# Optimization experiments

Hardware: AMD Instinct MI355X
Metric: run time of the kernel (lower is better)

## Reference

```python
import jax, jax.numpy as jnp
import numpy as np

FACTOR = 1.0
KERNEL = 3
PAD = 1
STRIDE = 1


def setup_inputs() -> dict:
    key = jax.random.key(0)
    ks = jax.random.split(key, 7)
    B_, Cin, Cout, L, CODE = 32, 128, 128, 4096, 2
    return {
        "input": jax.random.normal(ks[0], (B_, Cin, L), dtype=jnp.float32),
        "codes": jax.random.normal(ks[1], (B_, CODE, CODE), dtype=jnp.float32),
        "weight": jax.random.normal(ks[2], (Cout, Cin, KERNEL), dtype=jnp.float32) * 0.05,
        "A": jax.random.normal(ks[3], (Cin, CODE, KERNEL), dtype=jnp.float32) * 0.05,
        "B": jax.random.normal(ks[4], (Cout, CODE, KERNEL), dtype=jnp.float32) * 0.05,
        "bias": jax.random.normal(ks[5], (Cout,), dtype=jnp.float32) * 0.05,
        "bias_context": jax.random.normal(ks[6], (CODE, Cout), dtype=jnp.float32) * 0.05,
    }


def reference(input, codes, weight, A, B, bias, bias_context):
    # Hypernetwork-generated per-sample conv weights (low-rank via codes)
    w = jnp.einsum('ick,bcr->birk', A, codes)            # (b, in, code, k)
    context_w = jnp.einsum('birk,ork->boik', w, B)       # (b, out, in, k)
    combined_weight = weight + FACTOR * context_w        # (b, out, in, k)

    diag = jnp.diagonal(codes, axis1=-2, axis2=-1)       # (b, code)
    context_bias = diag @ bias_context                   # (b, out)
    combined_bias = bias + FACTOR * context_bias         # (b, out)

    # circular padding along spatial axis
    padded = jnp.pad(input, ((0, 0), (0, 0), (PAD, PAD)), mode='wrap')
    L_out = (input.shape[-1] + 2 * PAD - KERNEL) // STRIDE + 1
    # windowed view: (b, in, L_out, k) via k shifted slices (k is tiny, loop ok)
    windows = jnp.stack([padded[:, :, j:j + L_out * STRIDE:STRIDE] for j in range(KERNEL)], axis=-1)
    out = jnp.einsum('bihw,boiw->boh', windows, combined_weight)
    return out + combined_bias[..., None]
```

## Files before the change

kernel.cpp:

```cpp
#include <hip/hip_runtime.h>
#include <hip/hip_bf16.h>
#include <stdint.h>
#include <stddef.h>

#define L_LEN 4096
#define CIN   128
#define COUT  128
#define NB    32
#define KTOT  384
#define TN    128
#define ROWS  (TN + 2)

typedef __bf16 bf16x8 __attribute__((ext_vector_type(8)));
typedef float  f32x4  __attribute__((ext_vector_type(4)));

__device__ __forceinline__ uint16_t f2bf(float f) {
    union { float f; uint32_t u; } v; v.f = f;
    return (uint16_t)((v.u + 0x7fffu + ((v.u >> 16) & 1u)) >> 16);
}
__device__ __forceinline__ uint32_t pack2(float lo, float hi) {
    return (uint32_t)f2bf(lo) | ((uint32_t)f2bf(hi) << 16);
}

__global__ __launch_bounds__(256) void geps_combine(
    const float* __restrict__ codes, const float* __restrict__ weight,
    const float* __restrict__ Amat,  const float* __restrict__ Bmat,
    const float* __restrict__ bias,  const float* __restrict__ bias_ctx,
    uint16_t* __restrict__ Wc, float* __restrict__ cbias)
{
    int tid = blockIdx.x * 256 + threadIdx.x;
    if (tid < NB * COUT * KTOT) {
        int b   = tid / (COUT * KTOT);
        int rem = tid % (COUT * KTOT);
        int o   = rem / KTOT;
        int kp  = rem % KTOT;
        int k   = kp >> 7;
        int i   = kp & 127;
        float cw = 0.f;
        #pragma unroll
        for (int c = 0; c < 2; ++c) {
            float a = Amat[i * 6 + c * 3 + k];
            #pragma unroll
            for (int r = 0; r < 2; ++r)
                cw += a * codes[b * 4 + c * 2 + r] * Bmat[o * 6 + r * 3 + k];
        }
        float val = weight[o * 384 + i * 3 + k] + cw;
        Wc[tid] = f2bf(val);
    }
    if (tid < NB * COUT) {
        int b = tid >> 7, o = tid & 127;
        float cb = bias[o];
        #pragma unroll
        for (int c = 0; c < 2; ++c)
            cb += codes[b * 4 + c * 2 + c] * bias_ctx[c * 128 + o];
        cbias[tid] = cb;
    }
}

__global__ __launch_bounds__(256, 4) void geps_conv(
    const float* __restrict__ in, const uint16_t* __restrict__ Wc,
    const float* __restrict__ cbias, float* __restrict__ out)
{
    __shared__ uint16_t __attribute__((aligned(16))) Xt[ROWS * 128];
    __shared__ float cb[COUT];

    const int tid  = threadIdx.x;
    const int b    = blockIdx.y;
    const int h0   = blockIdx.x * TN;
    const int lane = tid & 63;
    const int wid  = tid >> 6;

    if (tid < COUT) cb[tid] = cbias[b * COUT + tid];

    const float* inb = in + (size_t)b * CIN * L_LEN;

    #pragma unroll
    for (int it = 0; it < 8; ++it) {
        int task = it * 256 + tid;
        int p    = task >> 5;
        int qd   = task & 31;
        const float* r0 = inb + (size_t)(2 * p) * L_LEN + h0 + 4 * qd;
        const float4 a  = *(const float4*)r0;
        const float4 c  = *(const float4*)(r0 + L_LEN);
        const int off   = (2 * p) & 7;
        const int pc    = p >> 2;
        const float av[4] = {a.x, a.y, a.z, a.w};
        const float cv[4] = {c.x, c.y, c.z, c.w};
        #pragma unroll
        for (int j = 0; j < 4; ++j) {
            int r = 1 + 4 * qd + j;
            int chunk = pc ^ (r & 15);
            *(uint32_t*)&Xt[r * 128 + (chunk << 3) + off] = pack2(av[j], cv[j]);
        }
    }
    if (tid < 128) {
        int p    = tid & 63;
        int side = tid >> 6;
        int r    = side ? (ROWS - 1) : 0;
        int gh   = (h0 - 1 + r) & (L_LEN - 1);
        float x0 = inb[(size_t)(2 * p)     * L_LEN + gh];
        float x1 = inb[(size_t)(2 * p + 1) * L_LEN + gh];
        int chunk = (p >> 2) ^ (r & 15);
        *(uint32_t*)&Xt[r * 128 + (chunk << 3) + ((2 * p) & 7)] = pack2(x0, x1);
    }

    const int mq  = (wid & 1) * 64;
    const int nq  = (wid >> 1) * 64;
    const int m16 = lane & 15;
    const int q   = lane >> 4;

    f32x4 acc[4][4];
    #pragma unroll
    for (int a = 0; a < 4; ++a)
        #pragma unroll
        for (int c = 0; c < 4; ++c) acc[a][c] = 0.0f;

    const uint16_t* WcB = Wc + (size_t)b * COUT * KTOT;

    __syncthreads();

    #pragma unroll
    for (int t = 0; t < 12; ++t) {
        const int k   = t >> 2;
        const int i0c = (t & 3) * 4;
        bf16x8 af[4], bf[4];
        #pragma unroll
        for (int mt = 0; mt < 4; ++mt) {
            int o = mq + mt * 16 + m16;
            af[mt] = *(const bf16x8*)(WcB + (size_t)o * KTOT + t * 32 + q * 8);
        }
        #pragma unroll
        for (int nt = 0; nt < 4; ++nt) {
            int r  = nq + nt * 16 + m16 + k;
            int ch = (i0c + q) ^ (r & 15);
            bf[nt] = *(const bf16x8*)&Xt[r * 128 + (ch << 3)];
        }
        #pragma unroll
        for (int mt = 0; mt < 4; ++mt)
            #pragma unroll
            for (int nt = 0; nt < 4; ++nt)
                acc[mt][nt] = __builtin_amdgcn_mfma_f32_16x16x32_bf16(
                    af[mt], bf[nt], acc[mt][nt], 0, 0, 0);
    }

    float* outb = out + (size_t)b * COUT * L_LEN + h0;
    #pragma unroll
    for (int mt = 0; mt < 4; ++mt) {
        #pragma unroll
        for (int reg = 0; reg < 4; ++reg) {
            int o = mq + mt * 16 + q * 4 + reg;
            float bv = cb[o];
            float* orow = outb + (size_t)o * L_LEN;
            #pragma unroll
            for (int nt = 0; nt < 4; ++nt) {
                int h = nq + nt * 16 + m16;
                orow[h] = acc[mt][nt][reg] + bv;
            }
        }
    }
}

extern "C" void kernel_launch(void* const* d_in, const int* in_sizes, int n_in,
                              void* d_out, int out_size, void* d_ws, size_t ws_size,
                              hipStream_t stream) {
    const float* input    = (const float*)d_in[0];
    const float* codes    = (const float*)d_in[1];
    const float* weight   = (const float*)d_in[2];
    const float* Amat     = (const float*)d_in[3];
    const float* Bmat     = (const float*)d_in[4];
    const float* bias     = (const float*)d_in[5];
    const float* bias_ctx = (const float*)d_in[6];
    float* out = (float*)d_out;

    uint16_t* Wc    = (uint16_t*)d_ws;
    float*    cbias = (float*)((char*)d_ws + (size_t)NB * COUT * KTOT * 2);

    geps_combine<<<dim3((NB * COUT * KTOT) / 256), 256, 0, stream>>>(
        codes, weight, Amat, Bmat, bias, bias_ctx, Wc, cbias);
    geps_conv<<<dim3(L_LEN / TN, NB), 256, 0, stream>>>(input, Wc, cbias, out);
}
```

Baseline: 145.6 us.

## Prefetch full weight slice into registers and repartition warps over output rows

Each wave now owns 32 output channels across all 128 positions rather than a 64x64 quadrant. All 12 K-steps of its weight fragments are loaded into registers up front, before the input staging, so global weight latency overlaps the LDS fill. The input staging loads four channel rows per thread and writes 64-bit LDS stores instead of 32-bit ones. Occupancy hint drops from 4 to 2 blocks per CU to make room for the larger register footprint. The risk is lower occupancy hiding less of the memory latency.

```diff
diff --git a/kernel.cpp b/kernel.cpp
--- a/kernel.cpp
+++ b/kernel.cpp
@@ -57,7 +57,7 @@
     }
 }
 
-__global__ __launch_bounds__(256, 4) void geps_conv(
+__global__ __launch_bounds__(256, 2) void geps_conv(
     const float* __restrict__ in, const uint16_t* __restrict__ Wc,
     const float* __restrict__ cbias, float* __restrict__ out)
 {
@@ -69,28 +69,47 @@
     const int h0   = blockIdx.x * TN;
     const int lane = tid & 63;
     const int wid  = tid >> 6;
+    const int m16  = lane & 15;
+    const int q    = lane >> 4;
+    const int mq   = wid * 32;
 
     if (tid < COUT) cb[tid] = cbias[b * COUT + tid];
 
-    const float* inb = in + (size_t)b * CIN * L_LEN;
+    const uint16_t* WcB = Wc + (size_t)b * COUT * KTOT;
+    const float*    inb = in + (size_t)b * CIN * L_LEN;
+
+    bf16x8 af[12][2];
+    #pragma unroll
+    for (int t = 0; t < 12; ++t)
+        #pragma unroll
+        for (int mt = 0; mt < 2; ++mt)
+            af[t][mt] = *(const bf16x8*)(WcB +
+                (size_t)(mq + mt * 16 + m16) * KTOT + t * 32 + q * 8);
 
     #pragma unroll
-    for (int it = 0; it < 8; ++it) {
+    for (int it = 0; it < 4; ++it) {
         int task = it * 256 + tid;
-        int p    = task >> 5;
+        int p4   = task >> 5;
         int qd   = task & 31;
-        const float* r0 = inb + (size_t)(2 * p) * L_LEN + h0 + 4 * qd;
-        const float4 a  = *(const float4*)r0;
-        const float4 c  = *(const float4*)(r0 + L_LEN);
-        const int off   = (2 * p) & 7;
-        const int pc    = p >> 2;
-        const float av[4] = {a.x, a.y, a.z, a.w};
-        const float cv[4] = {c.x, c.y, c.z, c.w};
+        const float* r0 = inb + (size_t)(4 * p4) * L_LEN + h0 + 4 * qd;
+        float4 a0 = *(const float4*)(r0);
+        float4 a1 = *(const float4*)(r0 + L_LEN);
+        float4 a2 = *(const float4*)(r0 + 2 * L_LEN);
+        float4 a3 = *(const float4*)(r0 + 3 * L_LEN);
+        const int off = (4 * p4) & 7;
+        const int pc  = p4 >> 1;
+        const float v0[4] = {a0.x, a0.y, a0.z, a0.w};
+        const float v1[4] = {a1.x, a1.y, a1.z, a1.w};
+        const float v2[4] = {a2.x, a2.y, a2.z, a2.w};
+        const float v3[4] = {a3.x, a3.y, a3.z, a3.w};
         #pragma unroll
         for (int j = 0; j < 4; ++j) {
-            int r = 1 + 4 * qd + j;
-            int chunk = pc ^ (r & 15);
-            *(uint32_t*)&Xt[r * 128 + (chunk << 3) + off] = pack2(av[j], cv[j]);
+            int r  = 1 + 4 * qd + j;
+            int ch = pc ^ (r & 15);
+            uint2 w;
+            w.x = pack2(v0[j], v1[j]);
+            w.y = pack2(v2[j], v3[j]);
+            *(uint2*)&Xt[r * 128 + (ch << 3) + off] = w;
         }
     }
     if (tid < 128) {
@@ -104,18 +123,11 @@
         *(uint32_t*)&Xt[r * 128 + (chunk << 3) + ((2 * p) & 7)] = pack2(x0, x1);
     }
 
-    const int mq  = (wid & 1) * 64;
-    const int nq  = (wid >> 1) * 64;
-    const int m16 = lane & 15;
-    const int q   = lane >> 4;
-
-    f32x4 acc[4][4];
+    f32x4 acc[2][8];
     #pragma unroll
-    for (int a = 0; a < 4; ++a)
+    for (int a = 0; a < 2; ++a)
         #pragma unroll
-        for (int c = 0; c < 4; ++c) acc[a][c] = 0.0f;
-
-    const uint16_t* WcB = Wc + (size_t)b * COUT * KTOT;
+        for (int c = 0; c < 8; ++c) acc[a][c] = 0.0f;
 
     __syncthreads();
 
@@ -123,37 +135,32 @@
     for (int t = 0; t < 12; ++t) {
         const int k   = t >> 2;
         const int i0c = (t & 3) * 4;
-        bf16x8 af[4], bf[4];
+        bf16x8 bf[8];
         #pragma unroll
-        for (int mt = 0; mt < 4; ++mt) {
-            int o = mq + mt * 16 + m16;
-            af[mt] = *(const bf16x8*)(WcB + (size_t)o * KTOT + t * 32 + q * 8);
-        }
-        #pragma unroll
-        for (int nt = 0; nt < 4; ++nt) {
-            int r  = nq + nt * 16 + m16 + k;
+        for (int nt = 0; nt < 8; ++nt) {
+            int r  = nt * 16 + m16 + k;
             int ch = (i0c + q) ^ (r & 15);
             bf[nt] = *(const bf16x8*)&Xt[r * 128 + (ch << 3)];
         }
         #pragma unroll
-        for (int mt = 0; mt < 4; ++mt)
+        for (int mt = 0; mt < 2; ++mt)
             #pragma unroll
-            for (int nt = 0; nt < 4; ++nt)
+            for (int nt = 0; nt < 8; ++nt)
                 acc[mt][nt] = __builtin_amdgcn_mfma_f32_16x16x32_bf16(
-                    af[mt], bf[nt], acc[mt][nt], 0, 0, 0);
+                    af[t][mt], bf[nt], acc[mt][nt], 0, 0, 0);
     }
 
     float* outb = out + (size_t)b * COUT * L_LEN + h0;
     #pragma unroll
-    for (int mt = 0; mt < 4; ++mt) {
+    for (int mt = 0; mt < 2; ++mt) {
         #pragma unroll
         for (int reg = 0; reg < 4; ++reg) {
             int o = mq + mt * 16 + q * 4 + reg;
             float bv = cb[o];
             float* orow = outb + (size_t)o * L_LEN;
             #pragma unroll
-            for (int nt = 0; nt < 4; ++nt) {
-                int h = nq + nt * 16 + m16;
+            for (int nt = 0; nt < 8; ++nt) {
+                int h = nt * 16 + m16;
                 orow[h] = acc[mt][nt][reg] + bv;
             }
         }
```

Result: faster. 140.7 us (-3.4%).

## Pre-swizzle combined weights into MFMA fragment order and shrink spatial tile

Applied to the files above, without the earlier changes.

The combine kernel now writes the per-sample bf16 weights directly in MFMA A-fragment order, so each lane in the conv kernel loads its fragment with one contiguous, fully coalesced 16-byte read. The conv tile shrinks from 128 to 32 positions, each warp owns 32 output channels over all 32 positions, and launch bounds allow 8 blocks per CU. The goal is more blocks, higher occupancy and cheaper weight loads. In exchange, each block reloads the whole weight slice for only 32 positions, so weight traffic goes up about fourfold and each warp gets less MFMA reuse.

```diff
diff --git a/kernel.cpp b/kernel.cpp
--- a/kernel.cpp
+++ b/kernel.cpp
@@ -8,7 +8,7 @@
 #define COUT  128
 #define NB    32
 #define KTOT  384
-#define TN    128
+#define TN    32
 #define ROWS  (TN + 2)
 
 typedef __bf16 bf16x8 __attribute__((ext_vector_type(8)));
@@ -26,16 +26,20 @@
     const float* __restrict__ codes, const float* __restrict__ weight,
     const float* __restrict__ Amat,  const float* __restrict__ Bmat,
     const float* __restrict__ bias,  const float* __restrict__ bias_ctx,
-    uint16_t* __restrict__ Wc, float* __restrict__ cbias)
+    uint16_t* __restrict__ Wc2, float* __restrict__ cbias)
 {
     int tid = blockIdx.x * 256 + threadIdx.x;
     if (tid < NB * COUT * KTOT) {
-        int b   = tid / (COUT * KTOT);
-        int rem = tid % (COUT * KTOT);
-        int o   = rem / KTOT;
-        int kp  = rem % KTOT;
-        int k   = kp >> 7;
-        int i   = kp & 127;
+        int j    = tid & 7;
+        int lane = (tid >> 3) & 63;
+        int og   = (tid >> 9) & 7;
+        int x    = tid >> 12;
+        int b    = x / 12;
+        int t    = x - b * 12;
+        int o    = og * 16 + (lane & 15);
+        int kap  = t * 32 + (lane >> 4) * 8 + j;
+        int k    = kap >> 7;
+        int i    = kap & 127;
         float cw = 0.f;
         #pragma unroll
         for (int c = 0; c < 2; ++c) {
@@ -44,8 +48,7 @@
             for (int r = 0; r < 2; ++r)
                 cw += a * codes[b * 4 + c * 2 + r] * Bmat[o * 6 + r * 3 + k];
         }
-        float val = weight[o * 384 + i * 3 + k] + cw;
-        Wc[tid] = f2bf(val);
+        Wc2[tid] = f2bf(weight[o * 384 + i * 3 + k] + cw);
     }
     if (tid < NB * COUT) {
         int b = tid >> 7, o = tid & 127;
@@ -57,8 +60,8 @@
     }
 }
 
-__global__ __launch_bounds__(256, 4) void geps_conv(
-    const float* __restrict__ in, const uint16_t* __restrict__ Wc,
+__global__ __launch_bounds__(256, 8) void geps_conv(
+    const float* __restrict__ in, const uint16_t* __restrict__ Wc2,
     const float* __restrict__ cbias, float* __restrict__ out)
 {
     __shared__ uint16_t __attribute__((aligned(16))) Xt[ROWS * 128];
@@ -69,16 +72,19 @@
     const int h0   = blockIdx.x * TN;
     const int lane = tid & 63;
     const int wid  = tid >> 6;
+    const int m16  = lane & 15;
+    const int q    = lane >> 4;
+    const int mq   = wid * 32;
 
     if (tid < COUT) cb[tid] = cbias[b * COUT + tid];
 
     const float* inb = in + (size_t)b * CIN * L_LEN;
 
     #pragma unroll
-    for (int it = 0; it < 8; ++it) {
+    for (int it = 0; it < 2; ++it) {
         int task = it * 256 + tid;
-        int p    = task >> 5;
-        int qd   = task & 31;
+        int p    = task >> 3;
+        int qd   = task & 7;
         const float* r0 = inb + (size_t)(2 * p) * L_LEN + h0 + 4 * qd;
         const float4 a  = *(const float4*)r0;
         const float4 c  = *(const float4*)(r0 + L_LEN);
@@ -88,9 +94,9 @@
         const float cv[4] = {c.x, c.y, c.z, c.w};
         #pragma unroll
         for (int j = 0; j < 4; ++j) {
-            int r = 1 + 4 * qd + j;
-            int chunk = pc ^ (r & 15);
-            *(uint32_t*)&Xt[r * 128 + (chunk << 3) + off] = pack2(av[j], cv[j]);
+            int r  = 1 + 4 * qd + j;
+            int ch = pc ^ (r & 15);
+            *(uint32_t*)&Xt[r * 128 + (ch << 3) + off] = pack2(av[j], cv[j]);
         }
     }
     if (tid < 128) {
@@ -100,62 +106,53 @@
         int gh   = (h0 - 1 + r) & (L_LEN - 1);
         float x0 = inb[(size_t)(2 * p)     * L_LEN + gh];
         float x1 = inb[(size_t)(2 * p + 1) * L_LEN + gh];
-        int chunk = (p >> 2) ^ (r & 15);
-        *(uint32_t*)&Xt[r * 128 + (chunk << 3) + ((2 * p) & 7)] = pack2(x0, x1);
+        int ch   = (p >> 2) ^ (r & 15);
+        *(uint32_t*)&Xt[r * 128 + (ch << 3) + ((2 * p) & 7)] = pack2(x0, x1);
     }
 
-    const int mq  = (wid & 1) * 64;
-    const int nq  = (wid >> 1) * 64;
-    const int m16 = lane & 15;
-    const int q   = lane >> 4;
+    f32x4 acc[2][2];
+    #pragma unroll
+    for (int a = 0; a < 2; ++a)
+        #pragma unroll
+        for (int c = 0; c < 2; ++c) acc[a][c] = 0.0f;
 
-    f32x4 acc[4][4];
-    #pragma unroll
-    for (int a = 0; a < 4; ++a)
-        #pragma unroll
-        for (int c = 0; c < 4; ++c) acc[a][c] = 0.0f;
-
-    const uint16_t* WcB = Wc + (size_t)b * COUT * KTOT;
+    const uint16_t* afb = Wc2 + ((((size_t)b * 12) * 8 + wid * 2) << 9) + lane * 8;
 
     __syncthreads();
 
-    #pragma unroll
+    #pragma unroll 2
     for (int t = 0; t < 12; ++t) {
         const int k   = t >> 2;
         const int i0c = (t & 3) * 4;
-        bf16x8 af[4], bf[4];
+        bf16x8 af[2], bf[2];
         #pragma unroll
-        for (int mt = 0; mt < 4; ++mt) {
-            int o = mq + mt * 16 + m16;
-            af[mt] = *(const bf16x8*)(WcB + (size_t)o * KTOT + t * 32 + q * 8);
-        }
+        for (int mt = 0; mt < 2; ++mt)
+            af[mt] = *(const bf16x8*)(afb + ((t * 8 + mt) << 9));
         #pragma unroll
-        for (int nt = 0; nt < 4; ++nt) {
-            int r  = nq + nt * 16 + m16 + k;
+        for (int nt = 0; nt < 2; ++nt) {
+            int r  = nt * 16 + m16 + k;
             int ch = (i0c + q) ^ (r & 15);
             bf[nt] = *(const bf16x8*)&Xt[r * 128 + (ch << 3)];
         }
         #pragma unroll
-        for (int mt = 0; mt < 4; ++mt)
+        for (int mt = 0; mt < 2; ++mt)
             #pragma unroll
-            for (int nt = 0; nt < 4; ++nt)
+            for (int nt = 0; nt < 2; ++nt)
                 acc[mt][nt] = __builtin_amdgcn_mfma_f32_16x16x32_bf16(
                     af[mt], bf[nt], acc[mt][nt], 0, 0, 0);
     }
 
     float* outb = out + (size_t)b * COUT * L_LEN + h0;
     #pragma unroll
-    for (int mt = 0; mt < 4; ++mt) {
+    for (int mt = 0; mt < 2; ++mt) {
         #pragma unroll
         for (int reg = 0; reg < 4; ++reg) {
             int o = mq + mt * 16 + q * 4 + reg;
             float bv = cb[o];
             float* orow = outb + (size_t)o * L_LEN;
             #pragma unroll
-            for (int nt = 0; nt < 4; ++nt) {
-                int h = nq + nt * 16 + m16;
-                orow[h] = acc[mt][nt][reg] + bv;
-            }
+            for (int nt = 0; nt < 2; ++nt)
+                orow[nt * 16 + m16] = acc[mt][nt][reg] + bv;
         }
     }
 }
@@ -172,10 +169,10 @@
     const float* bias_ctx = (const float*)d_in[6];
     float* out = (float*)d_out;
 
-    uint16_t* Wc    = (uint16_t*)d_ws;
+    uint16_t* Wc2   = (uint16_t*)d_ws;
     float*    cbias = (float*)((char*)d_ws + (size_t)NB * COUT * KTOT * 2);
 
     geps_combine<<<dim3((NB * COUT * KTOT) / 256), 256, 0, stream>>>(
-        codes, weight, Amat, Bmat, bias, bias_ctx, Wc, cbias);
-    geps_conv<<<dim3(L_LEN / TN, NB), 256, 0, stream>>>(input, Wc, cbias, out);
+        codes, weight, Amat, Bmat, bias, bias_ctx, Wc2, cbias);
+    geps_conv<<<dim3(L_LEN / TN, NB), 256, 0, stream>>>(input, Wc2, cbias, out);
 }
```

Result: slower. 154.6 us (+6.2%).

## Pre-transpose input to bf16 HxC layout and swap GEMM operand roles

Applied to the files above, without the earlier changes.

Adds a prep kernel that both converts the fp32 input into a bf16 transposed (L x Cin) buffer in workspace and writes the combined weights pre-swizzled into MFMA fragment order. The main GEMM then reads both operands straight from global memory with no LDS staging, swaps operand roles so that output stores are 16-byte vectors along L, and remaps blocks onto XCDs by batch. A fused fallback that keeps the LDS path runs when the workspace is too small. The extra pass costs a full read of the input and a write plus re-read of a half-size bf16 copy.

```diff
diff --git a/kernel.cpp b/kernel.cpp
--- a/kernel.cpp
+++ b/kernel.cpp
@@ -8,8 +8,7 @@
 #define COUT  128
 #define NB    32
 #define KTOT  384
-#define TN    128
-#define ROWS  (TN + 2)
+#define ROWS  130
 
 typedef __bf16 bf16x8 __attribute__((ext_vector_type(8)));
 typedef float  f32x4  __attribute__((ext_vector_type(4)));
@@ -22,92 +21,204 @@
     return (uint32_t)f2bf(lo) | ((uint32_t)f2bf(hi) << 16);
 }
 
-__global__ __launch_bounds__(256) void geps_combine(
+__global__ __launch_bounds__(256) void geps_prep(
+    const float* __restrict__ in,
     const float* __restrict__ codes, const float* __restrict__ weight,
     const float* __restrict__ Amat,  const float* __restrict__ Bmat,
     const float* __restrict__ bias,  const float* __restrict__ bias_ctx,
-    uint16_t* __restrict__ Wc, float* __restrict__ cbias)
+    uint16_t* __restrict__ Wc2, float* __restrict__ cbias,
+    uint16_t* __restrict__ xT, int t_blocks)
 {
-    int tid = blockIdx.x * 256 + threadIdx.x;
-    if (tid < NB * COUT * KTOT) {
-        int b   = tid / (COUT * KTOT);
-        int rem = tid % (COUT * KTOT);
-        int o   = rem / KTOT;
-        int kp  = rem % KTOT;
-        int k   = kp >> 7;
-        int i   = kp & 127;
-        float cw = 0.f;
-        #pragma unroll
-        for (int c = 0; c < 2; ++c) {
-            float a = Amat[i * 6 + c * 3 + k];
-            #pragma unroll
-            for (int r = 0; r < 2; ++r)
-                cw += a * codes[b * 4 + c * 2 + r] * Bmat[o * 6 + r * 3 + k];
-        }
-        float val = weight[o * 384 + i * 3 + k] + cw;
-        Wc[tid] = f2bf(val);
-    }
-    if (tid < NB * COUT) {
-        int b = tid >> 7, o = tid & 127;
-        float cb = bias[o];
-        #pragma unroll
-        for (int c = 0; c < 2; ++c)
-            cb += codes[b * 4 + c * 2 + c] * bias_ctx[c * 128 + o];
-        cbias[tid] = cb;
-    }
-}
-
-__global__ __launch_bounds__(256, 4) void geps_conv(
-    const float* __restrict__ in, const uint16_t* __restrict__ Wc,
+    __shared__ uint16_t __attribute__((aligned(16))) Xt[128 * 128];
+    const int tid = threadIdx.x;
+
+    if ((int)blockIdx.x < t_blocks) {
+        const int b  = blockIdx.x >> 5;
+        const int h0 = (blockIdx.x & 31) << 7;
+        const float* inb = in + ((size_t)b << 19);
+        #pragma unroll
+        for (int it = 0; it < 4; ++it) {
+            int task = it * 256 + tid;
+            int p4 = task >> 5, qd = task & 31;
+            const float* r0 = inb + (size_t)(p4 << 2) * L_LEN + h0 + (qd << 2);
+            float4 a0 = *(const float4*)(r0);
+            float4 a1 = *(const float4*)(r0 + L_LEN);
+            float4 a2 = *(const float4*)(r0 + 2 * L_LEN);
+            float4 a3 = *(const float4*)(r0 + 3 * L_LEN);
+            const int off = (p4 << 2) & 7, pc = p4 >> 1;
+            const float v0[4] = {a0.x, a0.y, a0.z, a0.w};
+            const float v1[4] = {a1.x, a1.y, a1.z, a1.w};
+            const float v2[4] = {a2.x, a2.y, a2.z, a2.w};
+            const float v3[4] = {a3.x, a3.y, a3.z, a3.w};
+            #pragma unroll
+            for (int j = 0; j < 4; ++j) {
+                int r  = (qd << 2) + j;
+                int ch = pc ^ (r & 15);
+                uint2 w; w.x = pack2(v0[j], v1[j]); w.y = pack2(v2[j], v3[j]);
+                *(uint2*)&Xt[r * 128 + (ch << 3) + off] = w;
+            }
+        }
+        __syncthreads();
+        uint16_t* dst = xT + (((size_t)b << 12) + h0) * 128;
+        #pragma unroll
+        for (int it = 0; it < 8; ++it) {
+            int task = it * 256 + tid;
+            int r = task >> 4, c = task & 15;
+            uint4 v = *(const uint4*)&Xt[r * 128 + ((c ^ (r & 15)) << 3)];
+            *(uint4*)&dst[(size_t)task << 3] = v;
+        }
+    } else {
+        int rb = blockIdx.x - t_blocks;
+        int e0 = (rb << 10) + (tid << 2);
+        int lane = (e0 >> 3) & 63, og = (e0 >> 9) & 7, x = e0 >> 12;
+        int b = x / 12, t = x - b * 12;
+        int o = (og << 4) + (lane & 15);
+        int kap0 = t * 32 + ((lane >> 4) << 3) + (e0 & 7);
+        uint16_t tmp[4];
+        #pragma unroll
+        for (int d = 0; d < 4; ++d) {
+            int kap = kap0 + d;
+            int k = kap >> 7, i = kap & 127;
+            float cw = 0.f;
+            #pragma unroll
+            for (int c = 0; c < 2; ++c) {
+                float a = Amat[i * 6 + c * 3 + k];
+                #pragma unroll
+                for (int r = 0; r < 2; ++r)
+                    cw += a * codes[b * 4 + c * 2 + r] * Bmat[o * 6 + r * 3 + k];
+            }
+            tmp[d] = f2bf(weight[o * 384 + i * 3 + k] + cw);
+        }
+        uint2 w;
+        w.x = (uint32_t)tmp[0] | ((uint32_t)tmp[1] << 16);
+        w.y = (uint32_t)tmp[2] | ((uint32_t)tmp[3] << 16);
+        *(uint2*)&Wc2[e0] = w;
+        if (rb < 16) {
+            int e = (rb << 8) + tid;
+            int bb = e >> 7, oo = e & 127;
+            float cb = bias[oo];
+            #pragma unroll
+            for (int c = 0; c < 2; ++c)
+                cb += codes[bb * 4 + c * 2 + c] * bias_ctx[c * 128 + oo];
+            cbias[e] = cb;
+        }
+    }
+}
+
+__global__ __launch_bounds__(256, 3) void geps_gemm(
+    const uint16_t* __restrict__ xT, const uint16_t* __restrict__ Wc2,
+    const float* __restrict__ cbias, float* __restrict__ out)
+{
+    const int id  = blockIdx.x;
+    const int xcd = id & 7, lin = id >> 3;
+    const int b   = (xcd << 2) + (lin >> 5);
+    const int h0  = (lin & 31) << 7;
+    const int tid = threadIdx.x, lane = tid & 63, wid = tid >> 6;
+    const int m16 = lane & 15, q = lane >> 4;
+    const int hq  = (wid & 1) << 6;
+    const int oq  = (wid >> 1) << 6;
+
+    const uint16_t* xb = xT  + ((size_t)b << 19);
+    const uint16_t* wb = Wc2 + (size_t)b * 49152;
+
+    float cbv[4];
+    #pragma unroll
+    for (int nt = 0; nt < 4; ++nt)
+        cbv[nt] = cbias[(b << 7) + oq + (nt << 4) + m16];
+
+    f32x4 acc[4][4];
+    #pragma unroll
+    for (int a = 0; a < 4; ++a)
+        #pragma unroll
+        for (int c = 0; c < 4; ++c) acc[a][c] = 0.0f;
+
+    #pragma unroll 2
+    for (int t = 0; t < 12; ++t) {
+        const int k1 = (t >> 2) - 1;
+        const int ib = ((t & 3) << 5) + (q << 3);
+        bf16x8 af[4], bfr[4];
+        #pragma unroll
+        for (int mt = 0; mt < 4; ++mt) {
+            int hr = (h0 + hq + (mt << 4) + m16 + k1) & (L_LEN - 1);
+            af[mt] = *(const bf16x8*)&xb[((size_t)hr << 7) + ib];
+        }
+        const uint16_t* wt = wb + ((size_t)(t * 8 + (oq >> 4)) << 9) + (lane << 3);
+        #pragma unroll
+        for (int nt = 0; nt < 4; ++nt)
+            bfr[nt] = *(const bf16x8*)(wt + ((size_t)nt << 9));
+        #pragma unroll
+        for (int mt = 0; mt < 4; ++mt)
+            #pragma unroll
+            for (int nt = 0; nt < 4; ++nt)
+                acc[mt][nt] = __builtin_amdgcn_mfma_f32_16x16x32_bf16(
+                    af[mt], bfr[nt], acc[mt][nt], 0, 0, 0);
+    }
+
+    float* ob = out + ((size_t)b << 7) * L_LEN;
+    #pragma unroll
+    for (int nt = 0; nt < 4; ++nt) {
+        const int o = oq + (nt << 4) + m16;
+        const float bv = cbv[nt];
+        #pragma unroll
+        for (int mt = 0; mt < 4; ++mt) {
+            const int h = h0 + hq + (mt << 4) + (q << 2);
+            f32x4 v = acc[mt][nt] + bv;
+            *(f32x4*)&ob[((size_t)o << 12) + h] = v;
+        }
+    }
+}
+
+__global__ __launch_bounds__(256, 3) void geps_conv_fused(
+    const float* __restrict__ in, const uint16_t* __restrict__ Wc2,
     const float* __restrict__ cbias, float* __restrict__ out)
 {
     __shared__ uint16_t __attribute__((aligned(16))) Xt[ROWS * 128];
-    __shared__ float cb[COUT];
-
-    const int tid  = threadIdx.x;
-    const int b    = blockIdx.y;
-    const int h0   = blockIdx.x * TN;
-    const int lane = tid & 63;
-    const int wid  = tid >> 6;
-
-    if (tid < COUT) cb[tid] = cbias[b * COUT + tid];
-
-    const float* inb = in + (size_t)b * CIN * L_LEN;
-
-    #pragma unroll
-    for (int it = 0; it < 8; ++it) {
+    const int id  = blockIdx.x;
+    const int xcd = id & 7, lin = id >> 3;
+    const int b   = (xcd << 2) + (lin >> 5);
+    const int h0  = (lin & 31) << 7;
+    const int tid = threadIdx.x, lane = tid & 63, wid = tid >> 6;
+    const int m16 = lane & 15, q = lane >> 4;
+    const int hq  = (wid & 1) << 6, oq = (wid >> 1) << 6;
+
+    const float* inb = in + ((size_t)b << 19);
+    #pragma unroll
+    for (int it = 0; it < 4; ++it) {
         int task = it * 256 + tid;
-        int p    = task >> 5;
-        int qd   = task & 31;
-        const float* r0 = inb + (size_t)(2 * p) * L_LEN + h0 + 4 * qd;
-        const float4 a  = *(const float4*)r0;
-        const float4 c  = *(const float4*)(r0 + L_LEN);
-        const int off   = (2 * p) & 7;
-        const int pc    = p >> 2;
-        const float av[4] = {a.x, a.y, a.z, a.w};
-        const float cv[4] = {c.x, c.y, c.z, c.w};
+        int p4 = task >> 5, qd = task & 31;
+        const float* r0 = inb + (size_t)(p4 << 2) * L_LEN + h0 + (qd << 2);
+        float4 a0 = *(const float4*)(r0);
+        float4 a1 = *(const float4*)(r0 + L_LEN);
+        float4 a2 = *(const float4*)(r0 + 2 * L_LEN);
+        float4 a3 = *(const float4*)(r0 + 3 * L_LEN);
+        const int off = (p4 << 2) & 7, pc = p4 >> 1;
+        const float v0[4] = {a0.x, a0.y, a0.z, a0.w};
+        const float v1[4] = {a1.x, a1.y, a1.z, a1.w};
+        const float v2[4] = {a2.x, a2.y, a2.z, a2.w};
+        const float v3[4] = {a3.x, a3.y, a3.z, a3.w};
         #pragma unroll
         for (int j = 0; j < 4; ++j) {
-            int r = 1 + 4 * qd + j;
-            int chunk = pc ^ (r & 15);
-            *(uint32_t*)&Xt[r * 128 + (chunk << 3) + off] = pack2(av[j], cv[j]);
+            int r  = 1 + (qd << 2) + j;
+            int ch = pc ^ (r & 15);
+            uint2 w; w.x = pack2(v0[j], v1[j]); w.y = pack2(v2[j], v3[j]);
+            *(uint2*)&Xt[r * 128 + (ch << 3) + off] = w;
         }
     }
     if (tid < 128) {
-        int p    = tid & 63;
-        int side = tid >> 6;
-        int r    = side ? (ROWS - 1) : 0;
-        int gh   = (h0 - 1 + r) & (L_LEN - 1);
-        float x0 = inb[(size_t)(2 * p)     * L_LEN + gh];
+        int p = tid & 63, side = tid >> 6;
+        int r = side ? (ROWS - 1) : 0;
+        int gh = (h0 - 1 + r) & (L_LEN - 1);
+        float x0 = inb[(size_t)(2 * p) * L_LEN + gh];
         float x1 = inb[(size_t)(2 * p + 1) * L_LEN + gh];
-        int chunk = (p >> 2) ^ (r & 15);
-        *(uint32_t*)&Xt[r * 128 + (chunk << 3) + ((2 * p) & 7)] = pack2(x0, x1);
-    }
-
-    const int mq  = (wid & 1) * 64;
-    const int nq  = (wid >> 1) * 64;
-    const int m16 = lane & 15;
-    const int q   = lane >> 4;
+        int ch = (p >> 2) ^ (r & 15);
+        *(uint32_t*)&Xt[r * 128 + (ch << 3) + ((2 * p) & 7)] = pack2(x0, x1);
+    }
+
+    const uint16_t* wb = Wc2 + (size_t)b * 49152;
+    float cbv[4];
+    #pragma unroll
+    for (int nt = 0; nt < 4; ++nt)
+        cbv[nt] = cbias[(b << 7) + oq + (nt << 4) + m16];
 
     f32x4 acc[4][4];
     #pragma unroll
@@ -115,47 +226,41 @@
         #pragma unroll
         for (int c = 0; c < 4; ++c) acc[a][c] = 0.0f;
 
-    const uint16_t* WcB = Wc + (size_t)b * COUT * KTOT;
-
     __syncthreads();
 
-    #pragma unroll
+    #pragma unroll 2
     for (int t = 0; t < 12; ++t) {
-        const int k   = t >> 2;
-        const int i0c = (t & 3) * 4;
-        bf16x8 af[4], bf[4];
+        const int k = t >> 2;
+        const int i0c = (t & 3) << 2;
+        bf16x8 af[4], bfr[4];
         #pragma unroll
         for (int mt = 0; mt < 4; ++mt) {
-            int o = mq + mt * 16 + m16;
-            af[mt] = *(const bf16x8*)(WcB + (size_t)o * KTOT + t * 32 + q * 8);
-        }
-        #pragma unroll
-        for (int nt = 0; nt < 4; ++nt) {
-            int r  = nq + nt * 16 + m16 + k;
+            int r  = hq + (mt << 4) + m16 + k;
             int ch = (i0c + q) ^ (r & 15);
-            bf[nt] = *(const bf16x8*)&Xt[r * 128 + (ch << 3)];
-        }
+            af[mt] = *(const bf16x8*)&Xt[r * 128 + (ch << 3)];
+        }
+        const uint16_t* wt = wb + ((size_t)(t * 8 + (oq >> 4)) << 9) + (lane << 3);
+        #pragma unroll
+        for (int nt = 0; nt < 4; ++nt)
+            bfr[nt] = *(const bf16x8*)(wt + ((size_t)nt << 9));
         #pragma unroll
         for (int mt = 0; mt < 4; ++mt)
             #pragma unroll
             for (int nt = 0; nt < 4; ++nt)
                 acc[mt][nt] = __builtin_amdgcn_mfma_f32_16x16x32_bf16(
-                    af[mt], bf[nt], acc[mt][nt], 0, 0, 0);
-    }
-
-    float* outb = out + (size_t)b * COUT * L_LEN + h0;
-    #pragma unroll
-    for (int mt = 0; mt < 4; ++mt) {
-        #pragma unroll
-        for (int reg = 0; reg < 4; ++reg) {
-            int o = mq + mt * 16 + q * 4 + reg;
-            float bv = cb[o];
-            float* orow = outb + (size_t)o * L_LEN;
-            #pragma unroll
-            for (int nt = 0; nt < 4; ++nt) {
-                int h = nq + nt * 16 + m16;
-                orow[h] = acc[mt][nt][reg] + bv;
-            }
+                    af[mt], bfr[nt], acc[mt][nt], 0, 0, 0);
+    }
+
+    float* ob = out + ((size_t)b << 7) * L_LEN;
+    #pragma unroll
+    for (int nt = 0; nt < 4; ++nt) {
+        const int o = oq + (nt << 4) + m16;
+        const float bv = cbv[nt];
+        #pragma unroll
+        for (int mt = 0; mt < 4; ++mt) {
+            const int h = h0 + hq + (mt << 4) + (q << 2);
+            f32x4 v = acc[mt][nt] + bv;
+            *(f32x4*)&ob[((size_t)o << 12) + h] = v;
         }
     }
 }
@@ -172,10 +277,24 @@
     const float* bias_ctx = (const float*)d_in[6];
     float* out = (float*)d_out;
 
-    uint16_t* Wc    = (uint16_t*)d_ws;
-    float*    cbias = (float*)((char*)d_ws + (size_t)NB * COUT * KTOT * 2);
-
-    geps_combine<<<dim3((NB * COUT * KTOT) / 256), 256, 0, stream>>>(
-        codes, weight, Amat, Bmat, bias, bias_ctx, Wc, cbias);
-    geps_conv<<<dim3(L_LEN / TN, NB), 256, 0, stream>>>(input, Wc, cbias, out);
-}
+    const size_t wc2_bytes = (size_t)NB * COUT * KTOT * 2;
+    const size_t cb_off    = wc2_bytes;
+    const size_t xt_off    = wc2_bytes + 16384;
+    const size_t xt_bytes  = (size_t)NB * L_LEN * CIN * 2;
+
+    uint16_t* Wc2   = (uint16_t*)d_ws;
+    float*    cbias = (float*)((char*)d_ws + cb_off);
+    uint16_t* xT    = (uint16_t*)((char*)d_ws + xt_off);
+
+    if (ws_size >= xt_off + xt_bytes) {
+        geps_prep<<<dim3(1024 + 1536), 256, 0, stream>>>(
+            input, codes, weight, Amat, Bmat, bias, bias_ctx,
+            Wc2, cbias, xT, 1024);
+        geps_gemm<<<dim3(1024), 256, 0, stream>>>(xT, Wc2, cbias, out);
+    } else {
+        geps_prep<<<dim3(1536), 256, 0, stream>>>(
+            input, codes, weight, Amat, Bmat, bias, bias_ctx,
+            Wc2, cbias, Wc2 , 0);
+        geps_conv_fused<<<dim3(1024), 256, 0, stream>>>(input, Wc2, cbias, out);
+    }
+}
```

After: 158.1 us. +8.6%, slower.
